# Performance work log

Measured on AMD Instinct MI355X. Metric: run time of the kernel, lower is better.

The kernel has to match this reference:

```python
import math
import jax, jax.numpy as jnp
import numpy as np

K_TOP = 8
D_HEAD = 32


def causal_topk_adjacency(x, K):
    # Binary adjacency: for each position t, top-K strictly-causal (j < t)
    # neighbours by dot-product similarity. Rows with < K valid positions
    # (e.g. t=0 has none) get only their valid entries (possibly zero rows).
    B, T, D = x.shape
    sim = jnp.einsum('btd,bsd->bts', x, x) / math.sqrt(D)  # (B,T,T)
    causal = jnp.tril(jnp.ones((T, T), dtype=bool), k=-1)   # j < t
    neg = jnp.finfo(sim.dtype).min
    sim_m = jnp.where(causal[None], sim, neg)
    vals, idx = jax.lax.top_k(sim_m, K)                      # (B,T,K)
    valid = (vals > neg).astype(x.dtype)
    b = jnp.arange(B)[:, None, None]
    t = jnp.arange(T)[None, :, None]
    A = jnp.zeros((B, T, T), x.dtype).at[b, t, idx].max(valid)
    return A


def setup_inputs() -> dict:
    key = jax.random.key(0)
    ks = jax.random.split(key, 3)
    B, T, D = 2, 4096, 1024
    x = jax.random.normal(ks[0], (B, T, D), dtype=jnp.float32)
    W_q = jax.random.normal(ks[1], (D_HEAD, D), dtype=jnp.float32) * (1.0 / math.sqrt(D))
    W_k = jax.random.normal(ks[2], (D_HEAD, D), dtype=jnp.float32) * (1.0 / math.sqrt(D))
    gain = jnp.ones((D,), dtype=jnp.float32)
    bias = jnp.zeros((D,), dtype=jnp.float32)
    log_mix = jnp.zeros((), dtype=jnp.float32)
    log_scale = jnp.zeros((), dtype=jnp.float32)
    return {"x": x, "W_q": W_q, "W_k": W_k, "gain": gain, "bias": bias,
            "log_mix": log_mix, "log_scale": log_scale}


def reference(x, W_q, W_k, gain, bias, log_mix, log_scale):
    B, T, D = x.shape
    mix = jax.nn.sigmoid(log_mix)
    scale = jax.nn.softplus(log_scale) + 0.01

    A = causal_topk_adjacency(x, K_TOP)                      # (B,T,T) binary

    q = jnp.einsum('btd,hd->bth', x, W_q)                    # (B,T,Dh)
    k = jnp.einsum('bsd,hd->bsh', x, W_k)
    score = jnp.einsum('bth,bsh->bts', q, k) / math.sqrt(D_HEAD)
    score = jnp.where(A < 0.5, -1e9, score)

    row_max = jax.lax.stop_gradient(jnp.max(score, axis=-1, keepdims=True))
    score = score - row_max
    attn = jax.nn.softmax(score, axis=-1)
    attn = jnp.nan_to_num(attn, nan=0.0)

    msg = jnp.einsum('bts,bsd->btd', attn, x)
    blended = mix * x + (1.0 - mix) * msg
    delta = jax.nn.gelu(blended * gain + bias, approximate=False) * scale
    return delta
```

## Files before the change

kernel.cpp:

```cpp
#include <hip/hip_runtime.h>
#include <math.h>

#define B 2
#define T 4096
#define D 1024
#define DH 32
#define TNB 32
#define NBLK 528
#define NK 12
#define CPR (32*NK)

typedef __bf16 bf16x8 __attribute__((ext_vector_type(8)));
typedef float f32x4 __attribute__((ext_vector_type(4)));

#define AS1 __attribute__((address_space(1)))
#define AS3 __attribute__((address_space(3)))

__device__ __forceinline__ unsigned mono32(float v) {
    unsigned u = __float_as_uint(v);
    u ^= ((unsigned)((int)u >> 31)) | 0x80000000u;
    return u;
}

__device__ __forceinline__ unsigned dpp_umax_bcast(unsigned v) {
    #define DPPMAX(CTRL) { unsigned t_ = (unsigned)__builtin_amdgcn_update_dpp(0, (int)v, CTRL, 0xF, 0xF, true); v = v > t_ ? v : t_; }
    DPPMAX(0x111) DPPMAX(0x112) DPPMAX(0x114) DPPMAX(0x118)
    DPPMAX(0x142) DPPMAX(0x143)
    #undef DPPMAX
    return (unsigned)__builtin_amdgcn_readlane((int)v, 63);
}
__device__ __forceinline__ float dpp_fsum_bcast(float v) {
    #define DPPADD(CTRL) { int t_ = __builtin_amdgcn_update_dpp(0, __float_as_int(v), CTRL, 0xF, 0xF, true); v += __int_as_float(t_); }
    DPPADD(0x111) DPPADD(0x112) DPPADD(0x114) DPPADD(0x118)
    DPPADD(0x142) DPPADD(0x143)
    #undef DPPADD
    return __int_as_float(__builtin_amdgcn_readlane(__float_as_int(v), 63));
}
__device__ __forceinline__ float dpp_gsum8(float p) {
    { int t_ = __builtin_amdgcn_update_dpp(0, __float_as_int(p), 0x0B1, 0xF, 0xF, true); p += __int_as_float(t_); }
    { int t_ = __builtin_amdgcn_update_dpp(0, __float_as_int(p), 0x04E, 0xF, 0xF, true); p += __int_as_float(t_); }
    { int t_ = __builtin_amdgcn_update_dpp(0, __float_as_int(p), 0x141, 0xF, 0xF, true); p += __int_as_float(t_); }
    return p;
}

__device__ __forceinline__ void merge12(const unsigned* a12, const unsigned* b12,
                                        unsigned* o12) {
    unsigned m16[16];
    #pragma unroll
    for (int i = 0; i < 16; ++i) {
        unsigned aa = (i < NK) ? a12[i] : 0u;
        unsigned bb = (15 - i < NK) ? b12[15 - i] : 0u;
        m16[i] = aa > bb ? aa : bb;
    }
    #pragma unroll
    for (int g = 8; g >= 1; g >>= 1) {
        #pragma unroll
        for (int i = 0; i < 16; ++i) {
            if (!(i & g)) {
                unsigned x0 = m16[i], x1 = m16[i + g];
                m16[i]     = x0 > x1 ? x0 : x1;
                m16[i + g] = x0 > x1 ? x1 : x0;
            }
        }
    }
    #pragma unroll
    for (int i = 0; i < NK; ++i) o12[i] = m16[i];
}

__global__ __launch_bounds__(256) void conv_kernel(const float* __restrict__ x,
        __bf16* __restrict__ xhi, __bf16* __restrict__ xlo)
{
    int i = (blockIdx.x * 256 + threadIdx.x) << 3;
    float4 a = *(const float4*)(x + i);
    float4 c = *(const float4*)(x + i + 4);
    float av[8] = {a.x, a.y, a.z, a.w, c.x, c.y, c.z, c.w};
    __bf16 h[8], l[8];
    #pragma unroll
    for (int j = 0; j < 8; ++j) {
        h[j] = (__bf16)av[j];
        l[j] = (__bf16)(av[j] - (float)h[j]);
    }
    *(float4*)(xhi + i) = *(float4*)h;
    *(float4*)(xlo + i) = *(float4*)l;
}

__global__ void mean_kernel(const float* __restrict__ x, float* __restrict__ meansum)
{
    int gid  = blockIdx.x;
    int b    = gid >> 6;
    int rem  = gid & 63;
    int dblk = rem >> 4;
    int tch  = rem & 15;
    int d = dblk * 256 + threadIdx.x;
    const float* xp = x + (b * T + tch * 256) * D + d;
    float s = 0.f;
    #pragma unroll 8
    for (int it = 0; it < 256; ++it) s += xp[it * D];
    atomicAdd(&meansum[(b << 10) + d], s);
}

__global__ __launch_bounds__(256) void qk_mfma_kernel(
        const __bf16* __restrict__ xhi, const __bf16* __restrict__ xlo,
        const __bf16* __restrict__ Whi, const __bf16* __restrict__ Wlo,
        float* __restrict__ qo, float* __restrict__ ko)
{
    __shared__ __align__(16) __bf16 stg[10240];
    __bf16* sAhi = stg;
    __bf16* sAlo = stg + 2560;
    __bf16* sBhi = stg + 5120;
    __bf16* sBlo = stg + 7680;

    int tid = threadIdx.x;
    int m0 = blockIdx.x << 6;
    int w = tid >> 6, lane = tid & 63;
    int fr = lane & 15, fq = lane >> 4;

    int arow = tid >> 2, aq = tid & 3;
    const __bf16* gAh = xhi + (size_t)(m0 + arow) * D + aq * 8;
    const __bf16* gAl = xlo + (size_t)(m0 + arow) * D + aq * 8;
    const __bf16* gBh = Whi + arow * D + aq * 8;
    const __bf16* gBl = Wlo + arow * D + aq * 8;

    f32x4 acc[4];
    #pragma unroll
    for (int j = 0; j < 4; ++j) acc[j] = (f32x4){0.f, 0.f, 0.f, 0.f};

    float4 a0 = *(const float4*)(gAh);
    float4 a1 = *(const float4*)(gAl);
    float4 b0 = *(const float4*)(gBh);
    float4 b1 = *(const float4*)(gBl);

    int sa = arow * 40 + aq * 8;

    for (int kc = 0; kc < 32; ++kc) {
        __syncthreads();
        *(float4*)(sAhi + sa) = a0;
        *(float4*)(sAlo + sa) = a1;
        *(float4*)(sBhi + sa) = b0;
        *(float4*)(sBlo + sa) = b1;
        __syncthreads();
        if (kc + 1 < 32) {
            int k0 = (kc + 1) << 5;
            a0 = *(const float4*)(gAh + k0);
            a1 = *(const float4*)(gAl + k0);
            b0 = *(const float4*)(gBh + k0);
            b1 = *(const float4*)(gBl + k0);
        }
        int r = (w << 4) + fr;
        bf16x8 fah = *(const bf16x8*)(sAhi + r * 40 + fq * 8);
        bf16x8 fal = *(const bf16x8*)(sAlo + r * 40 + fq * 8);
        bf16x8 fbh[4], fbl[4];
        #pragma unroll
        for (int j = 0; j < 4; ++j) {
            int rb = j * 16 + fr;
            fbh[j] = *(const bf16x8*)(sBhi + rb * 40 + fq * 8);
            fbl[j] = *(const bf16x8*)(sBlo + rb * 40 + fq * 8);
        }
        #pragma unroll
        for (int j = 0; j < 4; ++j) {
            acc[j] = __builtin_amdgcn_mfma_f32_16x16x32_bf16(fah, fbh[j], acc[j], 0, 0, 0);
            acc[j] = __builtin_amdgcn_mfma_f32_16x16x32_bf16(fah, fbl[j], acc[j], 0, 0, 0);
            acc[j] = __builtin_amdgcn_mfma_f32_16x16x32_bf16(fal, fbh[j], acc[j], 0, 0, 0);
        }
    }
    int grow0 = m0 + (w << 4) + (fq << 2);
    #pragma unroll
    for (int j = 0; j < 4; ++j) {
        int gn = j * 16 + fr;
        float* dst = (gn < 32) ? (qo + grow0 * DH + gn)
                               : (ko + grow0 * DH + gn - 32);
        dst[0]      = acc[j][0];
        dst[DH]     = acc[j][1];
        dst[2 * DH] = acc[j][2];
        dst[3 * DH] = acc[j][3];
    }
}

__global__ __launch_bounds__(256, 4) void topk_mfma_kernel(
        const __bf16* __restrict__ xhi, unsigned* __restrict__ pkey)
{
    __shared__ __align__(16) char smem[39680];
    __bf16* stg = (__bf16*)smem;
    float* Sbuf = (float*)smem;
    unsigned* kbuf = (unsigned*)(smem + 33024);

    int tid = threadIdx.x;
    int b = blockIdx.x / NBLK;
    int l = blockIdx.x - b * NBLK;
    int rt = (int)((sqrtf(8.f * l + 1.f) - 1.f) * 0.5f);
    while ((rt + 1) * (rt + 2) / 2 <= l) ++rt;
    while (rt * (rt + 1) / 2 > l) --rt;
    int ct = l - rt * (rt + 1) / 2;
    int r0 = rt << 7, c0 = ct << 7;
    int base = b * T;

    int w = tid >> 6, lane = tid & 63;
    int wr = (w >> 1) << 6, wc = (w & 1) << 6;
    bool active = !(rt == ct && w == 1);
    int fr = lane & 15, fq = lane >> 4;
    int fqs = (fq ^ ((fr >> 1) & 3)) << 3;

    int lrow = lane >> 2;
    int lcq = (((lane & 3) ^ ((lane >> 3) & 3)) << 3);
    const __bf16* gA = xhi + (size_t)(base + r0) * D;
    const __bf16* gB = xhi + (size_t)(base + c0) * D;
    const __bf16* gA0 = gA + (size_t)((w << 4) + lrow) * D + lcq;
    const __bf16* gA1 = gA0 + (size_t)64 * D;
    const __bf16* gB0 = gB + (size_t)((w << 4) + lrow) * D + lcq;
    const __bf16* gB1 = gB0 + (size_t)64 * D;

    f32x4 acc[4][4];
    #pragma unroll
    for (int i = 0; i < 4; ++i)
        #pragma unroll
        for (int j = 0; j < 4; ++j) acc[i][j] = (f32x4){0.f, 0.f, 0.f, 0.f};

#define ISSUE_TILE(BUFBASE, KO) do { \
    __bf16* bA_ = (BUFBASE); \
    __bf16* bB_ = bA_ + 4096; \
    __builtin_amdgcn_global_load_lds((const AS1 unsigned int*)(gA0 + (KO)), \
        (AS3 unsigned int*)(bA_ + (w << 9)), 16, 0, 0); \
    __builtin_amdgcn_global_load_lds((const AS1 unsigned int*)(gA1 + (KO)), \
        (AS3 unsigned int*)(bA_ + 2048 + (w << 9)), 16, 0, 0); \
    __builtin_amdgcn_global_load_lds((const AS1 unsigned int*)(gB0 + (KO)), \
        (AS3 unsigned int*)(bB_ + (w << 9)), 16, 0, 0); \
    __builtin_amdgcn_global_load_lds((const AS1 unsigned int*)(gB1 + (KO)), \
        (AS3 unsigned int*)(bB_ + 2048 + (w << 9)), 16, 0, 0); \
} while (0)

    ISSUE_TILE(stg, 0);
    ISSUE_TILE(stg + 8192, 32);

    for (int kc = 0; kc < 32; ++kc) {
        if (kc < 31) { asm volatile("s_waitcnt vmcnt(4)" ::: "memory"); }
        else         { asm volatile("s_waitcnt vmcnt(0)" ::: "memory"); }
        __builtin_amdgcn_s_barrier();
        asm volatile("" ::: "memory");
        if (active) {
            const __bf16* cA = stg + ((kc & 1) << 13);
            const __bf16* cB = cA + 4096;
            bf16x8 ah[4], bh[4];
            #pragma unroll
            for (int i = 0; i < 4; ++i) {
                int ar = wr + i * 16 + fr;
                ah[i] = *(const bf16x8*)(cA + ar * 32 + fqs);
                int bc = wc + i * 16 + fr;
                bh[i] = *(const bf16x8*)(cB + bc * 32 + fqs);
            }
            #pragma unroll
            for (int i = 0; i < 4; ++i)
                #pragma unroll
                for (int j = 0; j < 4; ++j)
                    acc[i][j] = __builtin_amdgcn_mfma_f32_16x16x32_bf16(ah[i], bh[j], acc[i][j], 0, 0, 0);
        }
        asm volatile("" ::: "memory");
        __builtin_amdgcn_s_barrier();
        asm volatile("" ::: "memory");
        if (kc + 2 < 32)
            ISSUE_TILE(stg + ((kc & 1) << 13), (kc + 2) << 5);
    }
#undef ISSUE_TILE

    int cr = fq << 2, cc = fr;
    #pragma unroll
    for (int phase = 0; phase < 2; ++phase) {
        __syncthreads();
        if ((w >> 1) == phase) {
            #pragma unroll
            for (int i = 0; i < 4; ++i)
                #pragma unroll
                for (int j = 0; j < 4; ++j) {
                    float* sp = Sbuf + (i * 16 + cr) * 129 + wc + j * 16 + cc;
                    sp[0]       = acc[i][j][0];
                    sp[129]     = acc[i][j][1];
                    sp[2 * 129] = acc[i][j][2];
                    sp[3 * 129] = acc[i][j][3];
                }
        }
        __syncthreads();
        if (tid < 128) {
            int row = tid & 63, half = tid >> 6;
            int gt = r0 + (phase << 6) + row;
            int cmax = gt - c0;
            if (cmax > 128) cmax = 128;
            if (cmax < 0) cmax = 0;
            int h0 = half << 6;
            int hmax = cmax < (h0 + 64) ? cmax : (h0 + 64);
            unsigned key[NK];
            #pragma unroll
            for (int i = 0; i < NK; ++i) key[i] = 0u;
            const float* Srow = Sbuf + row * 129;
            for (int cb = h0; cb < hmax; cb += 8) {
                float v[8];
                #pragma unroll
                for (int j = 0; j < 8; ++j) v[j] = Srow[cb + j];
                #pragma unroll
                for (int j = 0; j < 8; ++j) {
                    int c = cb + j;
                    unsigned u = mono32(v[j]);
                    unsigned tk = (c < hmax) ? ((u & 0xFFFFFF80u) | (unsigned)(127 - c)) : 0u;
                    #pragma unroll
                    for (int i = 0; i < NK; ++i) {
                        unsigned hi = key[i] > tk ? key[i] : tk;
                        unsigned lo = key[i] > tk ? tk : key[i];
                        key[i] = hi; tk = lo;
                    }
                }
            }
            #pragma unroll
            for (int i = 0; i < NK; ++i) kbuf[tid * 13 + i] = key[i];
        }
        __syncthreads();
        if (tid < 64) {
            unsigned a12[NK], b12[NK], o12[NK];
            #pragma unroll
            for (int i = 0; i < NK; ++i) {
                a12[i] = kbuf[tid * 13 + i];
                b12[i] = kbuf[(tid + 64) * 13 + i];
            }
            merge12(a12, b12, o12);
            int gt = r0 + (phase << 6) + tid;
            int ob = (base + gt) * CPR + ct * NK;
            #pragma unroll
            for (int i = 0; i < NK; ++i) {
                unsigned kk = o12[i];
                int gcol = c0 + 127 - (int)(kk & 127u);
                pkey[ob + i] = kk ? ((kk & 0xFFFFF000u) | (unsigned)(4095 - gcol)) : 0u;
            }
        }
    }
}

__global__ __launch_bounds__(256) void select_msg_kernel(const float* __restrict__ x,
        const float* __restrict__ q, const float* __restrict__ k,
        const float* __restrict__ meansum,
        const unsigned* __restrict__ pkey,
        const float* __restrict__ gain, const float* __restrict__ bias,
        const float* __restrict__ plm, const float* __restrict__ pls,
        float* __restrict__ out)
{
    int tid = threadIdx.x;
    int w = tid >> 6, lane = tid & 63;
    int rid = (blockIdx.x << 2) + w;
    int b = rid >> 12, t = rid & (T - 1);
    int ncand = NK * ((t + 127) >> 7);

    unsigned cv[6];
    #pragma unroll
    for (int u = 0; u < 6; ++u) {
        int cid = lane + (u << 6);
        cv[u] = (cid < ncand) ? pkey[(size_t)rid * CPR + cid] : 0u;
    }
    const float* xt = x + (size_t)rid * D;
    float4 xt4[4];
    #pragma unroll
    for (int c = 0; c < 4; ++c)
        xt4[c] = *(const float4*)(xt + (c << 8) + (lane << 2));

    unsigned skey[NK]; int sgid[NK];
    #pragma unroll
    for (int i = 0; i < NK; ++i) {
        unsigned m = cv[0];
        #pragma unroll
        for (int u = 1; u < 6; ++u) m = m > cv[u] ? m : cv[u];
        m = dpp_umax_bcast(m);
        skey[i] = m;
        sgid[i] = 4095 - (int)(m & 4095u);
        #pragma unroll
        for (int u = 0; u < 6; ++u) cv[u] = (cv[u] == m) ? 0u : cv[u];
    }

    float ex[NK];
    #pragma unroll
    for (int batch = 0; batch < 3; ++batch) {
        float4 rv[4][4];
        #pragma unroll
        for (int s = 0; s < 4; ++s) {
            int i = batch * 4 + s;
            int row = (skey[i] != 0u) ? sgid[i] : 0;
            const float* xj = x + (size_t)((b << 12) + row) * D;
            #pragma unroll
            for (int c = 0; c < 4; ++c)
                rv[s][c] = *(const float4*)(xj + (c << 8) + (lane << 2));
        }
        #pragma unroll
        for (int s = 0; s < 4; ++s) {
            float ss = 0.f;
            #pragma unroll
            for (int c = 0; c < 4; ++c)
                ss += xt4[c].x * rv[s][c].x + xt4[c].y * rv[s][c].y
                    + xt4[c].z * rv[s][c].z + xt4[c].w * rv[s][c].w;
            ex[batch * 4 + s] = dpp_fsum_bcast(ss);
        }
    }

    unsigned long long top8[8];
    #pragma unroll
    for (int r = 0; r < 8; ++r) top8[r] = 0ull;
    #pragma unroll
    for (int i = 0; i < NK; ++i) {
        unsigned u = mono32(ex[i]);
        unsigned long long t64 = (skey[i] != 0u)
            ? ((((unsigned long long)u) << 12) | (unsigned long long)(4095 - sgid[i]))
            : 0ull;
        #pragma unroll
        for (int r = 0; r < 8; ++r) {
            unsigned long long hi = (t64 > top8[r]) ? t64 : top8[r];
            unsigned long long lo = (t64 > top8[r]) ? top8[r] : t64;
            top8[r] = hi; t64 = lo;
        }
    }
    bool vld[8]; int bidx[8];
    #pragma unroll
    for (int i = 0; i < 8; ++i) {
        vld[i]  = top8[i] != 0ull;
        bidx[i] = 4095 - (int)(top8[i] & 4095ull);
    }

    int i8 = lane >> 3, e = lane & 7;
    unsigned long long kk = (i8 & 4)
        ? ((i8 & 2) ? ((i8 & 1) ? top8[7] : top8[6]) : ((i8 & 1) ? top8[5] : top8[4]))
        : ((i8 & 2) ? ((i8 & 1) ? top8[3] : top8[2]) : ((i8 & 1) ? top8[1] : top8[0]));
    bool v8 = kk != 0ull;
    int g8 = v8 ? (4095 - (int)(kk & 4095ull)) : 0;
    float4 qv = *(const float4*)(q + (size_t)rid * DH + (e << 2));
    float4 kv = *(const float4*)(k + (size_t)((b << 12) + g8) * DH + (e << 2));
    float p = qv.x * kv.x + qv.y * kv.y + qv.z * kv.z + qv.w * kv.w;
    p = dpp_gsum8(p);
    p *= 0.17677669529663687f;

    float sc[8];
    #pragma unroll
    for (int i = 0; i < 8; ++i)
        sc[i] = __int_as_float(__builtin_amdgcn_readlane(__float_as_int(p), i << 3));

    float m = -INFINITY; int cnt = 0;
    #pragma unroll
    for (int i = 0; i < 8; ++i)
        if (vld[i]) { ++cnt; if (sc[i] > m) m = sc[i]; }

    float wgt[8]; float Z = 0.f; int gsel[8];
    #pragma unroll
    for (int i = 0; i < 8; ++i) {
        wgt[i] = vld[i] ? expf(sc[i] - m) : 0.f;
        Z += wgt[i];
        gsel[i] = vld[i] ? ((b << 12) + bidx[i]) : (b << 12);
    }
    float invZ = (cnt > 0) ? 1.f / Z : 0.f;
    #pragma unroll
    for (int i = 0; i < 8; ++i) wgt[i] *= invZ;

    float mix   = 1.f / (1.f + expf(-plm[0]));
    float scale = log1pf(expf(pls[0])) + 0.01f;
    const float onemix = 1.f - mix;

    float4 msg4[4];
    if (cnt == 0) {
        #pragma unroll
        for (int c = 0; c < 4; ++c) {
            float4 ms = *(const float4*)(meansum + (b << 10) + (c << 8) + (lane << 2));
            msg4[c].x = ms.x * (1.f / (float)T); msg4[c].y = ms.y * (1.f / (float)T);
            msg4[c].z = ms.z * (1.f / (float)T); msg4[c].w = ms.w * (1.f / (float)T);
        }
    } else {
        #pragma unroll
        for (int c = 0; c < 4; ++c) msg4[c] = (float4){0.f, 0.f, 0.f, 0.f};
        #pragma unroll
        for (int g = 0; g < 2; ++g) {
            float4 rv[4][4];
            #pragma unroll
            for (int s = 0; s < 4; ++s) {
                const float* xj = x + (size_t)gsel[g * 4 + s] * D;
                #pragma unroll
                for (int c = 0; c < 4; ++c)
                    rv[s][c] = *(const float4*)(xj + (c << 8) + (lane << 2));
            }
            #pragma unroll
            for (int s = 0; s < 4; ++s) {
                float wi = wgt[g * 4 + s];
                #pragma unroll
                for (int c = 0; c < 4; ++c) {
                    msg4[c].x += wi * rv[s][c].x; msg4[c].y += wi * rv[s][c].y;
                    msg4[c].z += wi * rv[s][c].z; msg4[c].w += wi * rv[s][c].w;
                }
            }
        }
    }
    #pragma unroll
    for (int c = 0; c < 4; ++c) {
        int d0 = (c << 8) + (lane << 2);
        float4 g4 = *(const float4*)(gain + d0);
        float4 b4 = *(const float4*)(bias + d0);
        float4 xv = xt4[c];
        float zi[4] = {
            (mix * xv.x + onemix * msg4[c].x) * g4.x + b4.x,
            (mix * xv.y + onemix * msg4[c].y) * g4.y + b4.y,
            (mix * xv.z + onemix * msg4[c].z) * g4.z + b4.z,
            (mix * xv.w + onemix * msg4[c].w) * g4.w + b4.w };
        float4 o4;
        o4.x = 0.5f * zi[0] * (1.f + erff(zi[0] * 0.70710678118654752f)) * scale;
        o4.y = 0.5f * zi[1] * (1.f + erff(zi[1] * 0.70710678118654752f)) * scale;
        o4.z = 0.5f * zi[2] * (1.f + erff(zi[2] * 0.70710678118654752f)) * scale;
        o4.w = 0.5f * zi[3] * (1.f + erff(zi[3] * 0.70710678118654752f)) * scale;
        *(float4*)(out + (size_t)rid * D + d0) = o4;
    }
}

extern "C" void kernel_launch(void* const* d_in, const int* in_sizes, int n_in,
                              void* d_out, int out_size, void* d_ws, size_t ws_size,
                              hipStream_t stream)
{
    const float* x    = (const float*)d_in[0];
    const float* Wq   = (const float*)d_in[1];
    const float* Wk   = (const float*)d_in[2];
    const float* gain = (const float*)d_in[3];
    const float* bias = (const float*)d_in[4];
    const float* plm  = (const float*)d_in[5];
    const float* pls  = (const float*)d_in[6];
    float* out = (float*)d_out;

    float* ws      = (float*)d_ws;
    float* q       = ws;
    float* k       = ws + 262144;
    float* meansum = ws + 524288;
    unsigned* pkey = (unsigned*)(ws + 526336);
    __bf16* xhi    = (__bf16*)(ws + 3672064);
    __bf16* xlo    = xhi + (size_t)B * T * D;
    __bf16* Whi    = xlo + (size_t)B * T * D;
    __bf16* Wlo    = Whi + 64 * D;

    hipMemsetAsync(meansum, 0, 2048 * sizeof(float), stream);
    conv_kernel<<<B * T * D / 2048, 256, 0, stream>>>(x, xhi, xlo);
    conv_kernel<<<16, 256, 0, stream>>>(Wq, Whi, Wlo);
    conv_kernel<<<16, 256, 0, stream>>>(Wk, Whi + 32 * D, Wlo + 32 * D);
    mean_kernel<<<128, 256, 0, stream>>>(x, meansum);
    qk_mfma_kernel<<<B * T / 64, 256, 0, stream>>>(xhi, xlo, Whi, Wlo, q, k);
    topk_mfma_kernel<<<B * NBLK, 256, 0, stream>>>(xhi, pkey);
    select_msg_kernel<<<B * T / 4, 256, 0, stream>>>(x, q, k, meansum, pkey,
                                                     gain, bias, plm, pls, out);
}
```

Measured before the change: 274.1 us.

## Load B operand directly to registers, triple-buffer A, parallelize top-k selection across all waves

```diff
diff --git a/kernel.cpp b/kernel.cpp
--- a/kernel.cpp
+++ b/kernel.cpp
@@ -12,6 +12,7 @@
 
 typedef __bf16 bf16x8 __attribute__((ext_vector_type(8)));
 typedef float f32x4 __attribute__((ext_vector_type(4)));
+typedef unsigned u32x4 __attribute__((ext_vector_type(4)));
 
 #define AS1 __attribute__((address_space(1)))
 #define AS3 __attribute__((address_space(3)))
@@ -179,10 +180,9 @@
 __global__ __launch_bounds__(256, 4) void topk_mfma_kernel(
         const __bf16* __restrict__ xhi, unsigned* __restrict__ pkey)
 {
-    __shared__ __align__(16) char smem[39680];
+    __shared__ __align__(16) char smem[33024];
     __bf16* stg = (__bf16*)smem;
     float* Sbuf = (float*)smem;
-    unsigned* kbuf = (unsigned*)(smem + 33024);
 
     int tid = threadIdx.x;
     int b = blockIdx.x / NBLK;
@@ -203,11 +203,13 @@
     int lrow = lane >> 2;
     int lcq = (((lane & 3) ^ ((lane >> 3) & 3)) << 3);
     const __bf16* gA = xhi + (size_t)(base + r0) * D;
-    const __bf16* gB = xhi + (size_t)(base + c0) * D;
     const __bf16* gA0 = gA + (size_t)((w << 4) + lrow) * D + lcq;
     const __bf16* gA1 = gA0 + (size_t)64 * D;
-    const __bf16* gB0 = gB + (size_t)((w << 4) + lrow) * D + lcq;
-    const __bf16* gB1 = gB0 + (size_t)64 * D;
+
+    const __bf16* gBf = xhi + (size_t)(base + c0) * D + fq * 8;
+    size_t bOff[4];
+    #pragma unroll
+    for (int i = 0; i < 4; ++i) bOff[i] = (size_t)(wc + i * 16 + fr) * D;
 
     f32x4 acc[4][4];
     #pragma unroll
@@ -215,53 +217,62 @@
         #pragma unroll
         for (int j = 0; j < 4; ++j) acc[i][j] = (f32x4){0.f, 0.f, 0.f, 0.f};
 
-#define ISSUE_TILE(BUFBASE, KO) do { \
+#define ISSUE_A(BUFBASE, KO) do { \
     __bf16* bA_ = (BUFBASE); \
-    __bf16* bB_ = bA_ + 4096; \
     __builtin_amdgcn_global_load_lds((const AS1 unsigned int*)(gA0 + (KO)), \
         (AS3 unsigned int*)(bA_ + (w << 9)), 16, 0, 0); \
     __builtin_amdgcn_global_load_lds((const AS1 unsigned int*)(gA1 + (KO)), \
         (AS3 unsigned int*)(bA_ + 2048 + (w << 9)), 16, 0, 0); \
-    __builtin_amdgcn_global_load_lds((const AS1 unsigned int*)(gB0 + (KO)), \
-        (AS3 unsigned int*)(bB_ + (w << 9)), 16, 0, 0); \
-    __builtin_amdgcn_global_load_lds((const AS1 unsigned int*)(gB1 + (KO)), \
-        (AS3 unsigned int*)(bB_ + 2048 + (w << 9)), 16, 0, 0); \
 } while (0)
 
-    ISSUE_TILE(stg, 0);
-    ISSUE_TILE(stg + 8192, 32);
-
-    for (int kc = 0; kc < 32; ++kc) {
-        if (kc < 31) { asm volatile("s_waitcnt vmcnt(4)" ::: "memory"); }
-        else         { asm volatile("s_waitcnt vmcnt(0)" ::: "memory"); }
-        __builtin_amdgcn_s_barrier();
-        asm volatile("" ::: "memory");
-        if (active) {
-            const __bf16* cA = stg + ((kc & 1) << 13);
-            const __bf16* cB = cA + 4096;
-            bf16x8 ah[4], bh[4];
-            #pragma unroll
-            for (int i = 0; i < 4; ++i) {
-                int ar = wr + i * 16 + fr;
-                ah[i] = *(const bf16x8*)(cA + ar * 32 + fqs);
-                int bc = wc + i * 16 + fr;
-                bh[i] = *(const bf16x8*)(cB + bc * 32 + fqs);
-            }
-            #pragma unroll
-            for (int i = 0; i < 4; ++i)
-                #pragma unroll
-                for (int j = 0; j < 4; ++j)
-                    acc[i][j] = __builtin_amdgcn_mfma_f32_16x16x32_bf16(ah[i], bh[j], acc[i][j], 0, 0, 0);
-        }
-        asm volatile("" ::: "memory");
-        __builtin_amdgcn_s_barrier();
-        asm volatile("" ::: "memory");
-        if (kc + 2 < 32)
-            ISSUE_TILE(stg + ((kc & 1) << 13), (kc + 2) << 5);
-    }
-#undef ISSUE_TILE
+    bf16x8 bcur[4], bnxt[4];
+    ISSUE_A(stg, 0);
+    ISSUE_A(stg + 4096, 32);
+    #pragma unroll
+    for (int i = 0; i < 4; ++i)
+        bcur[i] = *(const bf16x8*)(gBf + bOff[i]);
+
+    int bsel = 0, isel = 2;
+#define K_STEP(KC, USE, PRE) do { \
+    asm volatile("s_waitcnt vmcnt(6)" ::: "memory"); \
+    __builtin_amdgcn_s_barrier(); \
+    asm volatile("" ::: "memory"); \
+    if ((KC) + 2 < 32) { \
+        ISSUE_A(stg + isel * 4096, ((KC) + 2) << 5); \
+        isel = (isel == 2) ? 0 : isel + 1; \
+    } \
+    if ((KC) + 1 < 32) { \
+        _Pragma("unroll") \
+        for (int i_ = 0; i_ < 4; ++i_) \
+            PRE[i_] = *(const bf16x8*)(gBf + bOff[i_] + (size_t)(((KC) + 1) << 5)); \
+    } \
+    if (active) { \
+        const __bf16* cA_ = stg + bsel * 4096; \
+        bf16x8 ah_[4]; \
+        _Pragma("unroll") \
+        for (int i_ = 0; i_ < 4; ++i_) { \
+            int ar_ = wr + i_ * 16 + fr; \
+            ah_[i_] = *(const bf16x8*)(cA_ + ar_ * 32 + fqs); \
+        } \
+        _Pragma("unroll") \
+        for (int i_ = 0; i_ < 4; ++i_) \
+            _Pragma("unroll") \
+            for (int j_ = 0; j_ < 4; ++j_) \
+                acc[i_][j_] = __builtin_amdgcn_mfma_f32_16x16x32_bf16(ah_[i_], USE[j_], acc[i_][j_], 0, 0, 0); \
+    } \
+    bsel = (bsel == 2) ? 0 : bsel + 1; \
+} while (0)
+
+    for (int kc2 = 0; kc2 < 16; ++kc2) {
+        int kc = kc2 << 1;
+        K_STEP(kc,     bcur, bnxt);
+        K_STEP(kc + 1, bnxt, bcur);
+    }
+#undef K_STEP
+#undef ISSUE_A
 
     int cr = fq << 2, cc = fr;
+    int q = lane >> 4;
     #pragma unroll
     for (int phase = 0; phase < 2; ++phase) {
         __syncthreads();
@@ -278,19 +289,21 @@
                 }
         }
         __syncthreads();
-        if (tid < 128) {
-            int row = tid & 63, half = tid >> 6;
-            int gt = r0 + (phase << 6) + row;
+        {
+            int sr = (w << 4) + (lane & 15);
+            int gt = r0 + (phase << 6) + sr;
             int cmax = gt - c0;
             if (cmax > 128) cmax = 128;
             if (cmax < 0) cmax = 0;
-            int h0 = half << 6;
-            int hmax = cmax < (h0 + 64) ? cmax : (h0 + 64);
+            int h0 = q << 5;
+            int hmax = cmax < (h0 + 32) ? cmax : (h0 + 32);
             unsigned key[NK];
             #pragma unroll
             for (int i = 0; i < NK; ++i) key[i] = 0u;
-            const float* Srow = Sbuf + row * 129;
-            for (int cb = h0; cb < hmax; cb += 8) {
+            const float* Srow = Sbuf + sr * 129;
+            #pragma unroll
+            for (int mb = 0; mb < 4; ++mb) {
+                int cb = h0 + (((mb + q) & 3) << 3);
                 float v[8];
                 #pragma unroll
                 for (int j = 0; j < 8; ++j) v[j] = Srow[cb + j];
@@ -308,24 +321,23 @@
                 }
             }
             #pragma unroll
-            for (int i = 0; i < NK; ++i) kbuf[tid * 13 + i] = key[i];
-        }
-        __syncthreads();
-        if (tid < 64) {
-            unsigned a12[NK], b12[NK], o12[NK];
-            #pragma unroll
-            for (int i = 0; i < NK; ++i) {
-                a12[i] = kbuf[tid * 13 + i];
-                b12[i] = kbuf[(tid + 64) * 13 + i];
+            for (int lvl = 0; lvl < 2; ++lvl) {
+                int xm = 16 << lvl;
+                unsigned o12[NK], m12[NK];
+                #pragma unroll
+                for (int i = 0; i < NK; ++i) o12[i] = __shfl_xor(key[i], xm);
+                merge12(key, o12, m12);
+                #pragma unroll
+                for (int i = 0; i < NK; ++i) key[i] = m12[i];
             }
-            merge12(a12, b12, o12);
-            int gt = r0 + (phase << 6) + tid;
-            int ob = (base + gt) * CPR + ct * NK;
-            #pragma unroll
-            for (int i = 0; i < NK; ++i) {
-                unsigned kk = o12[i];
-                int gcol = c0 + 127 - (int)(kk & 127u);
-                pkey[ob + i] = kk ? ((kk & 0xFFFFF000u) | (unsigned)(4095 - gcol)) : 0u;
+            if (q < 3) {
+                u32x4 ov;
+                #pragma unroll
+                for (int j = 0; j < 4; ++j) {
+                    unsigned k0 = (q == 0) ? key[j] : (q == 1) ? key[4 + j] : key[8 + j];
+                    ov[j] = k0 ? ((k0 & 0xFFFFF000u) | ((k0 & 127u) + (unsigned)(3968 - c0))) : 0u;
+                }
+                *(u32x4*)(pkey + (size_t)(base + gt) * CPR + ct * NK + (q << 2)) = ov;
             }
         }
     }
```

After: 296.1 us. 1.08x slower.
